# Kernel optimization log

Hardware: AMD Instinct MI355X
Metric: run time of the kernel (lower is better)

## Reference

```python
import jax, jax.numpy as jnp
import numpy as np

NUM_HEADS = 8
LN_EPS = 1e-5


def setup_inputs() -> dict:
    key = jax.random.key(0)
    ks = jax.random.split(key, 9)
    B, C, H, W = 8, 512, 32, 32
    s = 1.0 / np.sqrt(C)
    return {
        "f_curr": jax.random.normal(ks[0], (B, C, H, W), dtype=jnp.float32),
        "f_prev": jax.random.normal(ks[1], (B, C, H, W), dtype=jnp.float32),
        "f_next": jax.random.normal(ks[2], (B, C, H, W), dtype=jnp.float32),
        "Wq": jax.random.normal(ks[3], (C, C), dtype=jnp.float32) * s,
        "Wk": jax.random.normal(ks[4], (C, C), dtype=jnp.float32) * s,
        "Wv": jax.random.normal(ks[5], (C, C), dtype=jnp.float32) * s,
        "Wo": jax.random.normal(ks[6], (C, C), dtype=jnp.float32) * s,
        "gamma": jnp.ones((C,), dtype=jnp.float32),
        "beta": jnp.zeros((C,), dtype=jnp.float32),
    }


def _flatten(f):
    # [B,C,H,W] -> [B, H*W, C]
    B, C, H, W = f.shape
    return f.reshape(B, C, H * W).transpose(0, 2, 1)


def reference(f_curr, f_prev, f_next, Wq, Wk, Wv, Wo, gamma, beta):
    B, C, H, W = f_curr.shape
    N = H * W
    hd = C // NUM_HEADS
    scale = hd ** -0.5

    curr_flat = _flatten(f_curr)                              # [B,N,C]
    neigh_flat = jnp.concatenate([_flatten(f_prev), _flatten(f_next)], axis=1)  # [B,2N,C]

    # torch Linear (no bias): y = x @ W.T
    Q = curr_flat @ Wq.T                                      # [B,N,C]
    K = neigh_flat @ Wk.T                                     # [B,2N,C]
    V = neigh_flat @ Wv.T                                     # [B,2N,C]

    def split_heads(t, L):
        return t.reshape(B, L, NUM_HEADS, hd).transpose(0, 2, 1, 3)  # [B,h,L,hd]

    Qh = split_heads(Q, N)
    Kh = split_heads(K, 2 * N)
    Vh = split_heads(V, 2 * N)

    scores = jnp.einsum("bhnd,bhmd->bhnm", Qh, Kh) * scale    # [B,h,N,2N]
    attn = jax.nn.softmax(scores, axis=-1)
    out = jnp.einsum("bhnm,bhmd->bhnd", attn, Vh)             # [B,h,N,hd]

    out = out.transpose(0, 2, 1, 3).reshape(B, N, C)          # merge heads
    out = curr_flat + out @ Wo.T                              # residual

    # LayerNorm over channel dim
    mu = jnp.mean(out, axis=-1, keepdims=True)
    var = jnp.mean(jnp.square(out - mu), axis=-1, keepdims=True)
    out = (out - mu) * jax.lax.rsqrt(var + LN_EPS) * gamma + beta

    return out.transpose(0, 2, 1).reshape(B, C, H, W)
```

## Files before the change

### kernel.cpp

```cpp
#include <hip/hip_runtime.h>
#include <hip/hip_bf16.h>
#include <math.h>

#define NH 8
#define HD 64
#define CH 512
#define NT 1024
#define NB 8

typedef __bf16 bf16_t;
typedef bf16_t bf16x8 __attribute__((ext_vector_type(8)));
typedef bf16_t bf16x4 __attribute__((ext_vector_type(4)));
typedef float  f32x4  __attribute__((ext_vector_type(4)));
typedef float  f32x16 __attribute__((ext_vector_type(16)));
typedef unsigned u32x4 __attribute__((ext_vector_type(4)));

#define MFMA16(a, b, c) __builtin_amdgcn_mfma_f32_16x16x32_bf16((a), (b), (c), 0, 0, 0)
#define MFMA32(a, b, c) __builtin_amdgcn_mfma_f32_32x32x16_bf16((a), (b), (c), 0, 0, 0)
#define EXP2(x) __builtin_amdgcn_exp2f(x)

__device__ __forceinline__ void gload16(const void* g, void* l) {
    __builtin_amdgcn_global_load_lds(
        (const __attribute__((address_space(1))) void*)g,
        (__attribute__((address_space(3))) void*)l, 16, 0, 0);
}

__device__ __forceinline__ unsigned cvtpk(float lo, float hi) {
    unsigned r;
    asm("v_cvt_pk_bf16_f32 %0, %1, %2" : "=v"(r) : "v"(lo), "v"(hi));
    return r;
}

__device__ __forceinline__ void plswap(unsigned& a, unsigned& b) {
    asm("v_permlane32_swap_b32 %0, %1" : "+v"(a), "+v"(b));
}

__global__ __launch_bounds__(256) void prep_kernel(
    const float* __restrict__ fc, const float* __restrict__ fp,
    const float* __restrict__ fn, bf16_t* __restrict__ Xc,
    bf16_t* __restrict__ Xn)
{
    __shared__ __align__(16) bf16_t tile[64 * 64];
    const int t = threadIdx.x;
    const int y = blockIdx.y;
    const int b = y / 3, ft = y % 3;
    const int c0 = (blockIdx.x & 7) * 64;
    const int n0 = (blockIdx.x >> 3) * 64;

    const float* src; bf16_t* dst;
    if (ft == 0)      { src = fc + (size_t)b * CH * NT; dst = Xc + (size_t)b * NT * CH; }
    else if (ft == 1) { src = fp + (size_t)b * CH * NT; dst = Xn + (size_t)b * 2 * NT * CH; }
    else              { src = fn + (size_t)b * CH * NT; dst = Xn + (size_t)b * 2 * NT * CH + (size_t)NT * CH; }

    const int nb = t & 15, cb = t >> 4;
    float4 ld[4];
#pragma unroll
    for (int i = 0; i < 4; ++i)
        ld[i] = *(const float4*)(src + (size_t)(c0 + cb * 4 + i) * NT + n0 + nb * 4);
    const float* lf = (const float*)ld;
#pragma unroll
    for (int j = 0; j < 4; ++j) {
        int n = nb * 4 + j;
        int v = (n >> 2) & 14;
        bf16x4 wv = { (bf16_t)lf[0 * 4 + j], (bf16_t)lf[1 * 4 + j],
                      (bf16_t)lf[2 * 4 + j], (bf16_t)lf[3 * 4 + j] };
        *(bf16x4*)(tile + n * 64 + ((cb ^ v) * 4)) = wv;
    }
    __syncthreads();
#pragma unroll
    for (int i = 0; i < 2; ++i) {
        int gid = t + i * 256;
        int n = gid >> 3, c16 = gid & 7;
        int v = (n >> 2) & 14;
        bf16x8 val = *(const bf16x8*)(tile + n * 64 + (((2 * c16) ^ v) * 4));
        *(bf16x8*)(dst + (size_t)(n0 + n) * CH + c0 + c16 * 8) = val;
    }
}

__global__ __launch_bounds__(256) void wcvt_kernel(
    const float* __restrict__ Wq, const float* __restrict__ Wk,
    const float* __restrict__ Wv, const float* __restrict__ Wo,
    bf16_t* __restrict__ Wb, float* __restrict__ SQz)
{
    const int m = blockIdx.y;
    const float* src = (m == 0) ? Wq : (m == 1) ? Wk : (m == 2) ? Wv : Wo;
    bf16_t* dst = Wb + (size_t)m * CH * CH;
    int gid = blockIdx.x * 256 + threadIdx.x;
    float4 v = *(const float4*)(src + (size_t)gid * 4);
    bf16x4 o = { (bf16_t)v.x, (bf16_t)v.y, (bf16_t)v.z, (bf16_t)v.w };
    *(bf16x4*)(dst + (size_t)gid * 4) = o;
    if (m == 0 && blockIdx.x < 16) {
        f32x4 zz = {0.f, 0.f, 0.f, 0.f};
        *(f32x4*)(SQz + (size_t)(blockIdx.x * 256 + threadIdx.x) * 4) = zz;
    }
}

template <bool SWAP>
__device__ __forceinline__ void gemm_core(const bf16_t* __restrict__ A,
                                          const bf16_t* __restrict__ B,
                                          bf16_t* aT, bf16_t* bT,
                                          f32x4 acc[4][4])
{
    const int t = threadIdx.x, w = t >> 6, lane = t & 63;
    const int lid = lane & 15, quad = lane >> 4;
    const int wm = w >> 1, wn = w & 1;
    const int l4 = lane >> 2, k4 = lane & 3;

    for (int kt = 0; kt < 16; ++kt) {
        const int k0 = kt * 32;
        __syncthreads();
#pragma unroll
        for (int i = 0; i < 2; ++i) {
            int q = w * 2 + i;
            int row = q * 16 + l4;
            int kk = k4 ^ ((row >> 1) & 3);
            gload16(A + (size_t)row * CH + k0 + kk * 8, aT + q * 512);
            gload16(B + (size_t)row * CH + k0 + kk * 8, bT + q * 512);
        }
        __syncthreads();

        const bf16_t* mT = SWAP ? bT : aT;
        const bf16_t* nT = SWAP ? aT : bT;
        bf16x8 mf[4], nf[4];
#pragma unroll
        for (int i = 0; i < 4; ++i) {
            int row = wm * 64 + i * 16 + lid;
            int kw = quad ^ ((row >> 1) & 3);
            mf[i] = *(const bf16x8*)(mT + row * 32 + kw * 8);
        }
#pragma unroll
        for (int i = 0; i < 4; ++i) {
            int row = wn * 64 + i * 16 + lid;
            int kw = quad ^ ((row >> 1) & 3);
            nf[i] = *(const bf16x8*)(nT + row * 32 + kw * 8);
        }
#pragma unroll
        for (int mi = 0; mi < 4; ++mi)
#pragma unroll
            for (int ni = 0; ni < 4; ++ni)
                acc[mi][ni] = MFMA16(mf[mi], nf[ni], acc[mi][ni]);
    }
}

__global__ __launch_bounds__(256) void qkv_kernel(
    const bf16_t* __restrict__ Xc, const bf16_t* __restrict__ Xn,
    const bf16_t* __restrict__ Wb,
    bf16_t* __restrict__ Qn, bf16_t* __restrict__ Kn, bf16_t* __restrict__ Vt)
{
    __shared__ __align__(16) bf16_t aT[128 * 32];
    __shared__ __align__(16) bf16_t bT[128 * 32];
    const int bx = blockIdx.x, b = blockIdx.y;
    const int t = threadIdx.x, w = t >> 6, lane = t & 63;
    const int lid = lane & 15, quad = lane >> 4;
    const int wm = w >> 1, wn = w & 1;
    const float QSC = 0.125f * 1.44269504f;

    f32x4 acc[4][4] = {};

    if (bx < 96) {
        const bf16_t* A; const bf16_t* B; bf16_t* O; float scale;
        if (bx < 32) {
            int nt = bx >> 2, ct = bx & 3;
            A = Xc + (size_t)b * NT * CH + (size_t)nt * 128 * CH;
            B = Wb + (size_t)0 * CH * CH + (size_t)ct * 128 * CH;
            O = Qn + (size_t)b * NT * CH + (size_t)nt * 128 * CH + ct * 128;
            scale = QSC;
        } else {
            int j = bx - 32, nt = j >> 2, ct = j & 3;
            A = Xn + (size_t)b * 2 * NT * CH + (size_t)nt * 128 * CH;
            B = Wb + (size_t)1 * CH * CH + (size_t)ct * 128 * CH;
            O = Kn + (size_t)b * 2 * NT * CH + (size_t)nt * 128 * CH + ct * 128;
            scale = 1.0f;
        }
        gemm_core<false>(A, B, aT, bT, acc);
#pragma unroll
        for (int mi = 0; mi < 4; ++mi)
#pragma unroll
            for (int ni = 0; ni < 4; ++ni)
#pragma unroll
                for (int r = 0; r < 4; ++r) {
                    int n  = wm * 64 + mi * 16 + quad * 4 + r;
                    int co = wn * 64 + ni * 16 + lid;
                    O[(size_t)n * CH + co] = (bf16_t)(acc[mi][ni][r] * scale);
                }
    } else {
        int j = bx - 96, nt = j >> 2, ct = j & 3;
        const bf16_t* A = Xn + (size_t)b * 2 * NT * CH + (size_t)nt * 128 * CH;
        const bf16_t* B = Wb + (size_t)2 * CH * CH + (size_t)ct * 128 * CH;
        bf16_t* O = Vt + (size_t)b * CH * 2 * NT + (size_t)ct * 128 * 2 * NT + nt * 128;
        gemm_core<true>(A, B, aT, bT, acc);
#pragma unroll
        for (int mi = 0; mi < 4; ++mi)
#pragma unroll
            for (int ni = 0; ni < 4; ++ni)
#pragma unroll
                for (int r = 0; r < 4; ++r) {
                    int co_l  = wm * 64 + mi * 16 + quad * 4 + r;
                    int key_l = wn * 64 + ni * 16 + lid;
                    O[(size_t)co_l * (2 * NT) + key_l] = (bf16_t)acc[mi][ni][r];
                }
    }
}

__global__ __launch_bounds__(256, 2) void attn_kernel(
    const bf16_t* __restrict__ Qn, const bf16_t* __restrict__ Kn,
    const bf16_t* __restrict__ Vt, bf16_t* __restrict__ AOn)
{
    __shared__ __align__(16) char smem[55808];
    float*  const scr_all = (float*)smem;
    bf16_t* const obuf    = (bf16_t*)(smem + 36864);
    float*  const l_scr   = (float*)(smem + 55296);

    const int t = threadIdx.x;
    const int w = t >> 6, lane = t & 63;
    const int wq = w >> 1, wk = w & 1;
    const int l31 = lane & 31, h = lane >> 5;

    const int bid = blockIdx.x;
    const int xcd = bid & 7, ii = bid >> 3;
    const int grp = xcd * 8 + (ii >> 3);
    const int qt  = ii & 7;
    const int b = grp >> 3, hh = grp & 7;
    const int q0 = qt * 128;

    const bf16_t* Qb  = Qn + ((size_t)b * NT + q0) * CH + hh * HD;
    const bf16_t* Kb  = Kn + (size_t)b * 2 * NT * CH + hh * HD;
    const bf16_t* Vtb = Vt + ((size_t)b * CH + hh * HD) * (2 * NT);
    bf16_t* AOb = AOn + ((size_t)b * NT + q0) * CH + hh * HD;

    const bf16_t* Qrow = Qb  + (size_t)(wq * 64 + l31) * CH + h * 8;
    const bf16_t* Krow = Kb  + (size_t)(wk * 64 + l31) * CH + h * 8;
    const bf16_t* Vrow = Vtb + (size_t)l31 * (2 * NT) + wk * 64 + h * 8;

    bf16x8 qf[2][4];
#pragma unroll
    for (int nf = 0; nf < 2; ++nf)
#pragma unroll
        for (int ks = 0; ks < 4; ++ks)
            qf[nf][ks] = *(const bf16x8*)(Qrow + (size_t)nf * 32 * CH + ks * 16);

    f32x16 o[2][2] = {};
    float lpart[2] = {0.f, 0.f};

    for (int kt = 0; kt < 16; ++kt) {
        const size_t kb = (size_t)kt * 128;

        bf16x8 kf[2][4];
#pragma unroll
        for (int mf = 0; mf < 2; ++mf)
#pragma unroll
            for (int ks = 0; ks < 4; ++ks)
                kf[mf][ks] = *(const bf16x8*)(Krow + (kb + mf * 32) * CH + ks * 16);

        f32x16 s[2][2] = {};
        __builtin_amdgcn_s_setprio(1);
#pragma unroll
        for (int ks = 0; ks < 4; ++ks)
#pragma unroll
            for (int mf = 0; mf < 2; ++mf)
#pragma unroll
                for (int nf = 0; nf < 2; ++nf)
                    s[mf][nf] = MFMA32(kf[mf][ks], qf[nf][ks], s[mf][nf]);
        __builtin_amdgcn_s_setprio(0);

        bf16x8 vf[2][4];
#pragma unroll
        for (int df = 0; df < 2; ++df)
#pragma unroll
            for (int ks = 0; ks < 4; ++ks)
                vf[df][ks] = *(const bf16x8*)(Vrow + (size_t)df * 32 * (2 * NT) + kb + ks * 16);

#pragma unroll
        for (int mf = 0; mf < 2; ++mf) {
            bf16x8 pfrag[2][2];
#pragma unroll
            for (int nf = 0; nf < 2; ++nf) {
                float p[16];
#pragma unroll
                for (int r = 0; r < 16; ++r) p[r] = EXP2(s[mf][nf][r]);
                lpart[nf] += ((p[0] + p[1]) + (p[2] + p[3]))
                           + ((p[4] + p[5]) + (p[6] + p[7]))
                           + ((p[8] + p[9]) + (p[10] + p[11]))
                           + ((p[12] + p[13]) + (p[14] + p[15]));
                unsigned a0 = cvtpk(p[0], p[1]),   b0 = cvtpk(p[4], p[5]);
                unsigned a1 = cvtpk(p[2], p[3]),   b1 = cvtpk(p[6], p[7]);
                unsigned a2 = cvtpk(p[8], p[9]),   b2 = cvtpk(p[12], p[13]);
                unsigned a3 = cvtpk(p[10], p[11]), b3 = cvtpk(p[14], p[15]);
                plswap(a0, b0); plswap(a1, b1); plswap(a2, b2); plswap(a3, b3);
                u32x4 f0 = { a0, a1, b0, b1 };
                u32x4 f1 = { a2, a3, b2, b3 };
                pfrag[nf][0] = __builtin_bit_cast(bf16x8, f0);
                pfrag[nf][1] = __builtin_bit_cast(bf16x8, f1);
            }
            __builtin_amdgcn_s_setprio(1);
#pragma unroll
            for (int fi = 0; fi < 2; ++fi) {
                const int ks = mf * 2 + fi;
#pragma unroll
                for (int df = 0; df < 2; ++df)
#pragma unroll
                    for (int nf = 0; nf < 2; ++nf)
                        o[df][nf] = MFMA32(vf[df][ks], pfrag[nf][fi], o[df][nf]);
            }
            __builtin_amdgcn_s_setprio(0);
        }
    }

    float l2[2];
#pragma unroll
    for (int nf = 0; nf < 2; ++nf)
        l2[nf] = lpart[nf] + __shfl_xor(lpart[nf], 32);

    if (wk == 1) {
        float* scr = scr_all + wq * 4352;
#pragma unroll
        for (int df = 0; df < 2; ++df)
#pragma unroll
            for (int nf = 0; nf < 2; ++nf) {
                int qrow = nf * 32 + l31;
#pragma unroll
                for (int g = 0; g < 4; ++g) {
                    int d = df * 32 + 8 * g + 4 * h;
                    f32x4 v = { o[df][nf][4 * g + 0], o[df][nf][4 * g + 1],
                                o[df][nf][4 * g + 2], o[df][nf][4 * g + 3] };
                    *(f32x4*)(scr + qrow * 68 + d) = v;
                }
            }
        if (h == 0) {
            l_scr[wq * 64 + 0 * 32 + l31] = l2[0];
            l_scr[wq * 64 + 1 * 32 + l31] = l2[1];
        }
    }
    __syncthreads();

    if (wk == 0) {
        const float* scr = scr_all + wq * 4352;
        float inv[2];
#pragma unroll
        for (int nf = 0; nf < 2; ++nf)
            inv[nf] = 1.0f / (l2[nf] + l_scr[wq * 64 + nf * 32 + l31]);
#pragma unroll
        for (int df = 0; df < 2; ++df)
#pragma unroll
            for (int nf = 0; nf < 2; ++nf) {
                int qrow = nf * 32 + l31;
#pragma unroll
                for (int g = 0; g < 4; ++g) {
                    int d = df * 32 + 8 * g + 4 * h;
                    f32x4 part = *(const f32x4*)(scr + qrow * 68 + d);
                    bf16x4 ov = {
                        (bf16_t)((o[df][nf][4 * g + 0] + part.x) * inv[nf]),
                        (bf16_t)((o[df][nf][4 * g + 1] + part.y) * inv[nf]),
                        (bf16_t)((o[df][nf][4 * g + 2] + part.z) * inv[nf]),
                        (bf16_t)((o[df][nf][4 * g + 3] + part.w) * inv[nf]) };
                    int qg = wq * 64 + qrow;
                    *(bf16x4*)(obuf + qg * 72 + (d ^ (qg & 24))) = ov;
                }
            }
    }
    __syncthreads();

#pragma unroll
    for (int i = 0; i < 4; ++i) {
        int gid = t + i * 256;
        int qr = gid >> 3, c8 = (gid & 7) * 8;
        *(bf16x8*)(AOb + (size_t)qr * CH + c8) =
            *(const bf16x8*)(obuf + qr * 72 + (c8 ^ (qr & 24)));
    }
}

__global__ __launch_bounds__(256) void proj_kernel(
    const bf16_t* __restrict__ AOn, const bf16_t* __restrict__ Wb,
    const float* __restrict__ fc, float* __restrict__ Zt,
    float* __restrict__ Ssum, float* __restrict__ Ssq)
{
    __shared__ __align__(16) bf16_t aT[128 * 32];
    __shared__ __align__(16) bf16_t bT[128 * 32];
    const int bx = blockIdx.x, b = blockIdx.y;
    const int nt = bx >> 2, ct = bx & 3;
    const int t = threadIdx.x, w = t >> 6, lane = t & 63;
    const int lid = lane & 15, quad = lane >> 4;
    const int wm = w >> 1, wn = w & 1;

    const bf16_t* A = AOn + (size_t)b * NT * CH + (size_t)nt * 128 * CH;
    const bf16_t* B = Wb + (size_t)3 * CH * CH + (size_t)ct * 128 * CH;

    f32x4 acc[4][4] = {};
    gemm_core<true>(A, B, aT, bT, acc);

    const size_t bofs = (size_t)b * CH * NT;
    float sP[4] = {0.f, 0.f, 0.f, 0.f}, qP[4] = {0.f, 0.f, 0.f, 0.f};
#pragma unroll
    for (int mi = 0; mi < 4; ++mi)
#pragma unroll
        for (int ni = 0; ni < 4; ++ni)
#pragma unroll
            for (int r = 0; r < 4; ++r) {
                int co_l = wm * 64 + mi * 16 + quad * 4 + r;
                int n_l  = wn * 64 + ni * 16 + lid;
                size_t idx = bofs + (size_t)(ct * 128 + co_l) * NT + nt * 128 + n_l;
                float z = acc[mi][ni][r] + fc[idx];
                Zt[idx] = z;
                sP[ni] += z;
                qP[ni] += z * z;
            }
#pragma unroll
    for (int ni = 0; ni < 4; ++ni) {
        sP[ni] += __shfl_xor(sP[ni], 16);  sP[ni] += __shfl_xor(sP[ni], 32);
        qP[ni] += __shfl_xor(qP[ni], 16);  qP[ni] += __shfl_xor(qP[ni], 32);
    }
    __syncthreads();
    float* sRed = (float*)aT;
    float* qRed = sRed + 256;
    if (quad == 0) {
#pragma unroll
        for (int ni = 0; ni < 4; ++ni) {
            sRed[w * 64 + ni * 16 + lid] = sP[ni];
            qRed[w * 64 + ni * 16 + lid] = qP[ni];
        }
    }
    __syncthreads();
    if (t < 128) {
        float s = sRed[t] + sRed[128 + t];
        float q = qRed[t] + qRed[128 + t];
        atomicAdd(&Ssum[(size_t)b * NT + nt * 128 + t], s);
        atomicAdd(&Ssq [(size_t)b * NT + nt * 128 + t], q);
    }
}

__global__ __launch_bounds__(256) void apply_kernel(
    const float* __restrict__ Zt, const float* __restrict__ Ssum,
    const float* __restrict__ Ssq, const float* __restrict__ gamma,
    const float* __restrict__ beta, float* __restrict__ out)
{
    const int row = blockIdx.x;
    const int co = row & 511, b = row >> 9;
    const int t = threadIdx.x;
    const float g = gamma[co], be = beta[co];
    const size_t base = (size_t)row * NT + t * 4;
    f32x4 z  = *(const f32x4*)(Zt + base);
    f32x4 S  = *(const f32x4*)(Ssum + (size_t)b * NT + t * 4);
    f32x4 Q2 = *(const f32x4*)(Ssq  + (size_t)b * NT + t * 4);
    f32x4 o;
#pragma unroll
    for (int c = 0; c < 4; ++c) {
        float mu  = S[c] * (1.0f / 512.0f);
        float var = Q2[c] * (1.0f / 512.0f) - mu * mu;
        float rs  = rsqrtf(var + 1e-5f);
        o[c] = (z[c] - mu) * rs * g + be;
    }
    *(f32x4*)(out + base) = o;
}

extern "C" void kernel_launch(void* const* d_in, const int* in_sizes, int n_in,
                              void* d_out, int out_size, void* d_ws, size_t ws_size,
                              hipStream_t stream)
{
    (void)in_sizes; (void)n_in; (void)out_size; (void)ws_size;
    const float* fc    = (const float*)d_in[0];
    const float* fp    = (const float*)d_in[1];
    const float* fn    = (const float*)d_in[2];
    const float* Wq    = (const float*)d_in[3];
    const float* Wk    = (const float*)d_in[4];
    const float* Wv    = (const float*)d_in[5];
    const float* Wo    = (const float*)d_in[6];
    const float* gamma = (const float*)d_in[7];
    const float* beta  = (const float*)d_in[8];
    float* out = (float*)d_out;

    char* ws = (char*)d_ws;
    bf16_t* Xn  = (bf16_t*)(ws);
    bf16_t* Qn  = (bf16_t*)(ws + 16777216);
    bf16_t* Kn  = (bf16_t*)(ws + 25165824);
    bf16_t* Xc  = (bf16_t*)(ws + 41943040);
    bf16_t* AOn = Xc;
    bf16_t* Vt  = (bf16_t*)(ws + 50331648);
    bf16_t* Wb  = (bf16_t*)(ws + 67108864);
    float*  Ssum = (float*)(ws + 69206016);
    float*  Ssq  = (float*)(ws + 69238784);
    float*  Zt  = (float*)(ws);

    prep_kernel<<<dim3(128, 24), 256, 0, stream>>>(fc, fp, fn, Xc, Xn);
    wcvt_kernel<<<dim3(256, 4), 256, 0, stream>>>(Wq, Wk, Wv, Wo, Wb, Ssum);
    qkv_kernel<<<dim3(160, 8), 256, 0, stream>>>(Xc, Xn, Wb, Qn, Kn, Vt);
    attn_kernel<<<dim3(512), 256, 0, stream>>>(Qn, Kn, Vt, AOn);
    proj_kernel<<<dim3(32, 8), 256, 0, stream>>>(AOn, Wb, fc, Zt, Ssum, Ssq);
    apply_kernel<<<4096, 256, 0, stream>>>(Zt, Ssum, Ssq, gamma, beta, out);
}
```

Baseline: 230.6 us.

## Stage K/V tiles through double-buffered swizzled LDS with async global-to-LDS loads

Attention now loads K and V tiles once per block into XOR-swizzled LDS with global_load_lds, double-buffered so the next tile is fetched while the current one is computed. Before, each wave read its own K/V fragments straight from global memory. The goal is to cut redundant global traffic, since waves sharing wk read the same keys, and to hide load latency. In exchange, LDS grows to 64KB, which may limit occupancy to 2 blocks per CU, and a barrier is added per key tile.

```diff
diff --git a/kernel.cpp b/kernel.cpp
--- a/kernel.cpp
+++ b/kernel.cpp
@@ -206,7 +206,11 @@
     const bf16_t* __restrict__ Qn, const bf16_t* __restrict__ Kn,
     const bf16_t* __restrict__ Vt, bf16_t* __restrict__ AOn)
 {
-    __shared__ __align__(16) char smem[55808];
+    __shared__ __align__(16) char smem[65536];
+    bf16_t* const kbuf0 = (bf16_t*)smem;
+    bf16_t* const kbuf1 = (bf16_t*)(smem + 16384);
+    bf16_t* const vbuf0 = (bf16_t*)(smem + 32768);
+    bf16_t* const vbuf1 = (bf16_t*)(smem + 49152);
     float*  const scr_all = (float*)smem;
     bf16_t* const obuf    = (bf16_t*)(smem + 36864);
     float*  const l_scr   = (float*)(smem + 55296);
@@ -228,10 +232,22 @@
     const bf16_t* Vtb = Vt + ((size_t)b * CH + hh * HD) * (2 * NT);
     bf16_t* AOb = AOn + ((size_t)b * NT + q0) * CH + hh * HD;
 
-    const bf16_t* Qrow = Qb  + (size_t)(wq * 64 + l31) * CH + h * 8;
-    const bf16_t* Krow = Kb  + (size_t)(wk * 64 + l31) * CH + h * 8;
-    const bf16_t* Vrow = Vtb + (size_t)l31 * (2 * NT) + wk * 64 + h * 8;
-
+#define STAGE_KV(kbn, kw, vw)                                                  \
+    {                                                                          \
+        _Pragma("unroll")                                                      \
+        for (int i = 0; i < 4; ++i) {                                          \
+            int ck = w * 64 + i * 256 + lane;                                  \
+            int kr = ck >> 3, kg = ck & 7;                                     \
+            gload16(Kb + (size_t)((kbn) + kr) * CH + ((kg ^ (kr & 7)) * 8),    \
+                    (kw) + (w * 64 + i * 256) * 8);                            \
+            int cv = ck;                                                       \
+            int vr = cv >> 4, vg = cv & 15;                                    \
+            gload16(Vtb + (size_t)vr * (2 * NT) + (kbn) + ((vg ^ (vr & 15)) * 8), \
+                    (vw) + (w * 64 + i * 256) * 8);                            \
+        }                                                                      \
+    }
+
+    const bf16_t* Qrow = Qb + (size_t)(wq * 64 + l31) * CH + h * 8;
     bf16x8 qf[2][4];
 #pragma unroll
     for (int nf = 0; nf < 2; ++nf)
@@ -239,45 +255,48 @@
         for (int ks = 0; ks < 4; ++ks)
             qf[nf][ks] = *(const bf16x8*)(Qrow + (size_t)nf * 32 * CH + ks * 16);
 
+    STAGE_KV(0, kbuf0, vbuf0);
+    __syncthreads();
+
     f32x16 o[2][2] = {};
     float lpart[2] = {0.f, 0.f};
 
+    const int swk = l31 & 7;
+    const int swv = l31 & 15;
+
     for (int kt = 0; kt < 16; ++kt) {
-        const size_t kb = (size_t)kt * 128;
-
-        bf16x8 kf[2][4];
-#pragma unroll
-        for (int mf = 0; mf < 2; ++mf)
+        const int cur = kt & 1;
+        const bf16_t* const kr_buf = cur ? kbuf1 : kbuf0;
+        const bf16_t* const vr_buf = cur ? vbuf1 : vbuf0;
+        bf16_t* const kw_buf = cur ? kbuf0 : kbuf1;
+        bf16_t* const vw_buf = cur ? vbuf0 : vbuf1;
+
+        if (kt < 15)
+            STAGE_KV((kt + 1) * 128, kw_buf, vw_buf);
+
+#pragma unroll
+        for (int mf = 0; mf < 2; ++mf) {
+            const int krow = wk * 64 + mf * 32 + l31;
+            bf16x8 kfm[4];
 #pragma unroll
             for (int ks = 0; ks < 4; ++ks)
-                kf[mf][ks] = *(const bf16x8*)(Krow + (kb + mf * 32) * CH + ks * 16);
-
-        f32x16 s[2][2] = {};
-        __builtin_amdgcn_s_setprio(1);
-#pragma unroll
-        for (int ks = 0; ks < 4; ++ks)
-#pragma unroll
-            for (int mf = 0; mf < 2; ++mf)
+                kfm[ks] = *(const bf16x8*)(kr_buf + krow * 64 + (((ks * 2 + h) ^ swk) * 8));
+
+            f32x16 s[2] = {};
+            __builtin_amdgcn_s_setprio(1);
+#pragma unroll
+            for (int ks = 0; ks < 4; ++ks)
 #pragma unroll
                 for (int nf = 0; nf < 2; ++nf)
-                    s[mf][nf] = MFMA32(kf[mf][ks], qf[nf][ks], s[mf][nf]);
-        __builtin_amdgcn_s_setprio(0);
-
-        bf16x8 vf[2][4];
-#pragma unroll
-        for (int df = 0; df < 2; ++df)
-#pragma unroll
-            for (int ks = 0; ks < 4; ++ks)
-                vf[df][ks] = *(const bf16x8*)(Vrow + (size_t)df * 32 * (2 * NT) + kb + ks * 16);
-
-#pragma unroll
-        for (int mf = 0; mf < 2; ++mf) {
+                    s[nf] = MFMA32(kfm[ks], qf[nf][ks], s[nf]);
+            __builtin_amdgcn_s_setprio(0);
+
             bf16x8 pfrag[2][2];
 #pragma unroll
             for (int nf = 0; nf < 2; ++nf) {
                 float p[16];
 #pragma unroll
-                for (int r = 0; r < 16; ++r) p[r] = EXP2(s[mf][nf][r]);
+                for (int r = 0; r < 16; ++r) p[r] = EXP2(s[nf][r]);
                 lpart[nf] += ((p[0] + p[1]) + (p[2] + p[3]))
                            + ((p[4] + p[5]) + (p[6] + p[7]))
                            + ((p[8] + p[9]) + (p[10] + p[11]))
@@ -292,19 +311,29 @@
                 pfrag[nf][0] = __builtin_bit_cast(bf16x8, f0);
                 pfrag[nf][1] = __builtin_bit_cast(bf16x8, f1);
             }
+
             __builtin_amdgcn_s_setprio(1);
 #pragma unroll
             for (int fi = 0; fi < 2; ++fi) {
                 const int ks = mf * 2 + fi;
+                bf16x8 av[2];
+#pragma unroll
+                for (int df = 0; df < 2; ++df) {
+                    int vrow = df * 32 + l31;
+                    av[df] = *(const bf16x8*)(vr_buf + vrow * 128 +
+                             (((wk * 8 + ks * 2 + h) ^ swv) * 8));
+                }
 #pragma unroll
                 for (int df = 0; df < 2; ++df)
 #pragma unroll
                     for (int nf = 0; nf < 2; ++nf)
-                        o[df][nf] = MFMA32(vf[df][ks], pfrag[nf][fi], o[df][nf]);
+                        o[df][nf] = MFMA32(av[df], pfrag[nf][fi], o[df][nf]);
             }
             __builtin_amdgcn_s_setprio(0);
         }
-    }
+        __syncthreads();
+    }
+#undef STAGE_KV
 
     float l2[2];
 #pragma unroll
```

Result: faster. 208.0 us (-9.8%).
